# Kernel tuning notes

Hardware: AMD Instinct MI355X
Metric: run time of the kernel (lower is better)

Reference implementation:

```python
import jax, jax.numpy as jnp
import numpy as np

# dims: Q queries, K hops (topk), N relation groups, M padded nodes/group
Q, K, N, M = 64, 2, 32, 64
E, D, R, S = 256, 1024, 200, 8192  # embs_size, model_size, n_rel, seq positions


def setup_inputs() -> dict:
    key = jax.random.key(0)
    ks = jax.random.split(key, 10)
    hidden_states = jax.random.normal(ks[0], (S, D), jnp.float32)
    nodes = jax.random.normal(ks[1], (Q, K, N, M, E), jnp.float32)
    # ragged groups: zero-pad beyond a random valid length (mirrors F.pad + stack)
    lengths = jax.random.randint(ks[2], (Q, K, N), 1, M + 1)
    valid = jnp.arange(M)[None, None, None, :] < lengths[..., None]
    nodes = nodes * valid[..., None]
    prob_idx = jax.random.randint(ks[3], (Q, K, N), 0, R)
    gnn_idx = jnp.arange(Q, dtype=jnp.int32)          # gnn_mask positions
    rel_idx = jnp.arange(Q, dtype=jnp.int32) + Q      # rel_mask positions (disjoint)
    sc = lambda fan: float(1.0 / np.sqrt(fan))
    u = lambda k, shp, fan: jax.random.uniform(k, shp, jnp.float32, -sc(fan), sc(fan))
    Wc = u(ks[4], (D, R), D); bc = jnp.zeros((R,), jnp.float32)
    Wq = u(ks[5], (D, D), D); bq = jnp.zeros((D,), jnp.float32)
    Wn = u(ks[6], (E, D), E); bn = jnp.zeros((D,), jnp.float32)
    Wg = u(ks[7], (E, D), E); bg = jnp.zeros((D,), jnp.float32)
    return {"hidden_states": hidden_states, "nodes": nodes, "prob_idx": prob_idx,
            "gnn_idx": gnn_idx, "rel_idx": rel_idx,
            "Wc": Wc, "bc": bc, "Wq": Wq, "bq": bq,
            "Wn": Wn, "bn": bn, "Wg": Wg, "bg": bg}


def reference(hidden_states, nodes, prob_idx, gnn_idx, rel_idx,
              Wc, bc, Wq, bq, Wn, bn, Wg, bg):
    Qn, Kn, Nn, Mn, En = nodes.shape
    # classification_head: Linear + Softmax over relations
    rel_prob = jax.nn.softmax(hidden_states[rel_idx] @ Wc + bc, axis=1)  # [Q,R]
    # gather per-group relation probabilities (extract_values_from_tensor)
    probs = jnp.take_along_axis(rel_prob, prob_idx.reshape(Qn, Kn * Nn), axis=1)
    probs = probs.reshape(Qn, Kn, Nn)                                     # [Q,K,N]
    # mask from first feature of padded node embeddings (as in calculate_scores)
    mask = nodes[..., 0] != 0                                             # [Q,K,N,M]
    # query_reprj and nodes_reprj (Linear + Tanh)
    gq = jnp.tanh(hidden_states[gnn_idx] @ Wq + bq)                       # [Q,D]
    gn = jnp.tanh(jnp.einsum('qknme,ed->qknmd', nodes, Wn) + bn)          # [Q,K,N,M,D]
    dots = jnp.einsum('qknmd,qd->qknm', gn, gq)                           # [Q,K,N,M]
    attn = jax.nn.softmax(dots, axis=3)            # softmax over nodes within group
    logits = attn * probs[..., None] / 0.1         # scale by group prob / temperature
    # global softmax over all (group, node) slots per (query, hop)
    wa = jax.nn.softmax(logits.reshape(Qn, Kn, Nn * Mn), axis=-1)
    wa = wa.reshape(Qn, Kn, Nn, Mn)
    wa = jnp.where(mask, wa, 0.0)
    # weighted mean over the flattened N*M slots, then mean over topk hops
    mean_emb = jnp.mean(nodes * wa[..., None], axis=(2, 3))               # [Q,K,E]
    pooled = mean_emb.mean(axis=1)                                        # [Q,E]
    out = jnp.tanh(pooled @ Wg + bg)                                      # gnn_reprj
    return hidden_states.at[gnn_idx].add(out)
```

## Files before the change

### kernel.cpp

```cpp
#include <hip/hip_runtime.h>
#include <hip/hip_bf16.h>
#include <math.h>

#define QDIM 64
#define KDIM 2
#define NDIM 32
#define MDIM 64
#define EDIM 256
#define DDIM 1024
#define RDIM 200
#define SDIM 8192
#define GCOUNT (QDIM * KDIM * NDIM)

typedef short short8_t __attribute__((ext_vector_type(8)));
typedef float f32x4 __attribute__((ext_vector_type(4)));

__device__ __forceinline__ float tanh_c(float x) {
    float e = __expf(2.0f * x);
    return 1.0f - 2.0f * __builtin_amdgcn_rcpf(1.0f + e);
}

__device__ __forceinline__ uint32_t f2bf(float f) {
    uint32_t u = __float_as_uint(f);
    return (u + 0x7fffu + ((u >> 16) & 1u)) >> 16;
}
__device__ __forceinline__ float bf2f(uint16_t h) {
    return __uint_as_float(((uint32_t)h) << 16);
}

__global__ __launch_bounds__(256) void prologue_kernel(
    const float* __restrict__ hs, float* __restrict__ out,
    const float* __restrict__ Wn, short* __restrict__ wnpk,
    const int* __restrict__ gnn_idx, const float* __restrict__ Wq,
    const float* __restrict__ bq, float* __restrict__ gqo,
    const int* __restrict__ rel_idx, const float* __restrict__ Wc,
    const float* __restrict__ bc, float* __restrict__ rel_prob,
    const float* __restrict__ nodes, int* __restrict__ nvarr) {
    const int b = blockIdx.x, t = threadIdx.x;
    __shared__ float row[DDIM];
    __shared__ float arr[256];

    if (b < 2048) {
        const float4* src = (const float4*)hs;
        float4* dst = (float4*)out;
        int i = b * 256 + t;
#pragma unroll
        for (int r = 0; r < 4; ++r) dst[i + r * 524288] = src[i + r * 524288];
    } else if (b < 2176) {
        int tid = (b - 2048) * 256 + t;
        int lane = tid & 63, ks = (tid >> 6) & 7, ntg = tid >> 9;
        int low = lane & 15, hi = lane >> 4;
        short8_t o;
#pragma unroll
        for (int j = 0; j < 8; ++j) {
            int k = ks * 32 + hi * 8 + j;
            int d = ntg * 16 + low;
            o[j] = (short)f2bf(Wn[(size_t)k * DDIM + d]);
        }
        *(short8_t*)(wnpk + (size_t)tid * 8) = o;
    } else if (b < 2432) {
        int bb = b - 2176;
        int q = bb >> 2, seg = bb & 3;
        const float* src = hs + (size_t)gnn_idx[q] * DDIM;
        for (int i = t; i < DDIM; i += 256) row[i] = src[i];
        __syncthreads();
        int d = seg * 256 + t;
        float a = bq[d];
#pragma unroll 8
        for (int k = 0; k < DDIM; ++k) a += row[k] * Wq[(size_t)k * DDIM + d];
        gqo[(size_t)q * DDIM + d] = tanh_c(a);
    } else if (b < 2496) {
        int q = b - 2432;
        const float* src = hs + (size_t)rel_idx[q] * DDIM;
        for (int i = t; i < DDIM; i += 256) row[i] = src[i];
        __syncthreads();
        float lg = -INFINITY;
        if (t < RDIM) {
            float a = bc[t];
            for (int k = 0; k < DDIM; ++k) a += row[k] * Wc[(size_t)k * RDIM + t];
            lg = a;
        }
        arr[t] = lg;
        __syncthreads();
        for (int s = 128; s > 0; s >>= 1) {
            if (t < s) arr[t] = fmaxf(arr[t], arr[t + s]);
            __syncthreads();
        }
        float mx = arr[0];
        __syncthreads();
        float ex = (t < RDIM) ? __expf(lg - mx) : 0.0f;
        arr[t] = ex;
        __syncthreads();
        for (int s = 128; s > 0; s >>= 1) {
            if (t < s) arr[t] += arr[t + s];
            __syncthreads();
        }
        float sm = arr[0];
        if (t < RDIM) rel_prob[q * RDIM + t] = ex / sm;
    } else {
        int g = (b - 2496) * 4 + (t >> 6);
        int lane = t & 63;
        float f0 = nodes[(size_t)g * (MDIM * EDIM) + (size_t)lane * EDIM];
        unsigned long long mk = __ballot(f0 != 0.0f);
        if (lane == 0) nvarr[g] = __popcll(mk);
    }
}

struct SharedBufs {
    alignas(16) char ldsbuf[MDIM * EDIM * 2];
    float part[4][MDIM];
    float cqp[4];
    float lv[MDIM];
};

template <int MT>
__device__ __forceinline__ void phase1_body(
    SharedBufs* sb, int g, int q, const float* __restrict__ nodes,
    const short* __restrict__ wnpk, const float* __restrict__ bn,
    const float* __restrict__ gq, const float* __restrict__ rel_prob,
    const int* __restrict__ prob_idx, float* __restrict__ gvec,
    float* __restrict__ gden, float* __restrict__ gmx) {
    const int t = threadIdx.x;
    const int lane = t & 63, w = t >> 6;
    const int low = lane & 15, hi = lane >> 4;
    constexpr int NS = MT * 16;
    constexpr int TAIL = 64 - NS;

    {
        const float4* src = (const float4*)(nodes + (size_t)g * (MDIM * EDIM));
#pragma unroll
        for (int i = 0; i < MT * 4; ++i) {
            int idx4 = i * 256 + t;
            float4 v = src[idx4];
            int m = idx4 >> 6;
            int byteoff = (m * 512 + (idx4 & 63) * 8) ^ ((m & 7) << 4);
            uint32_t w0 = f2bf(v.x) | (f2bf(v.y) << 16);
            uint32_t w1 = f2bf(v.z) | (f2bf(v.w) << 16);
            *(uint2*)(sb->ldsbuf + byteoff) = make_uint2(w0, w1);
        }
    }
    __syncthreads();

    short8_t af[MT][8];
#pragma unroll
    for (int mt = 0; mt < MT; ++mt)
#pragma unroll
        for (int ks = 0; ks < 8; ++ks) {
            int rrow = mt * 16 + low;
            int byteoff = (rrow * 512 + ks * 64 + hi * 16) ^ ((low & 7) << 4);
            af[mt][ks] = *(const short8_t*)(sb->ldsbuf + byteoff);
        }

    float dacc[MT][4];
#pragma unroll
    for (int mt = 0; mt < MT; ++mt)
#pragma unroll
        for (int jj = 0; jj < 4; ++jj) dacc[mt][jj] = 0.f;

    float cpart = 0.f;
    const float* gqrow = gq + (size_t)q * DDIM;
    for (int nt = 0; nt < 16; ++nt) {
        const int ntg = w * 16 + nt;
        const int d = ntg * 16 + low;
        float gqv = gqrow[d];
        float bnv = bn[d];
        cpart += tanh_c(bnv) * gqv;
        f32x4 acc[MT];
#pragma unroll
        for (int mt = 0; mt < MT; ++mt) acc[mt] = (f32x4){0.f, 0.f, 0.f, 0.f};
        const short8_t* bp = (const short8_t*)(wnpk) + ((size_t)ntg * 8 * 64 + lane);
#pragma unroll
        for (int ks = 0; ks < 8; ++ks) {
            short8_t bf = bp[ks * 64];
#pragma unroll
            for (int mt = 0; mt < MT; ++mt)
                acc[mt] = __builtin_amdgcn_mfma_f32_16x16x32_bf16(af[mt][ks], bf, acc[mt], 0, 0, 0);
        }
#pragma unroll
        for (int mt = 0; mt < MT; ++mt)
#pragma unroll
            for (int jj = 0; jj < 4; ++jj)
                dacc[mt][jj] += tanh_c(acc[mt][jj] + bnv) * gqv;
    }

#pragma unroll
    for (int mt = 0; mt < MT; ++mt)
#pragma unroll
        for (int jj = 0; jj < 4; ++jj) {
            float v = dacc[mt][jj];
            v += __shfl_xor(v, 1);
            v += __shfl_xor(v, 2);
            v += __shfl_xor(v, 4);
            v += __shfl_xor(v, 8);
            if (low == 0) sb->part[w][mt * 16 + hi * 4 + jj] = v;
        }
    {
        float cw = cpart;
#pragma unroll
        for (int off = 32; off > 0; off >>= 1) cw += __shfl_xor(cw, off);
        if (lane == 0) sb->cqp[w] = cw;
    }
    __syncthreads();

    if (t < 64) {
        float cq = 0.25f * (sb->cqp[0] + sb->cqp[1] + sb->cqp[2] + sb->cqp[3]);
        float dv = (t < NS) ? (sb->part[0][t] + sb->part[1][t] + sb->part[2][t] + sb->part[3][t])
                            : -INFINITY;
        float mx = dv;
#pragma unroll
        for (int off = 32; off > 0; off >>= 1) mx = fmaxf(mx, __shfl_xor(mx, off));
        if (TAIL > 0) mx = fmaxf(mx, cq);
        float ex = (t < NS) ? __expf(dv - mx) : 0.0f;
        float sm = ex;
#pragma unroll
        for (int off = 32; off > 0; off >>= 1) sm += __shfl_xor(sm, off);
        float ext = __expf(cq - mx);
        sm += (float)TAIL * ext;
        float pr = rel_prob[(size_t)q * RDIM + prob_idx[g]];
        float attn = ex / sm;
        float lgv = (t < NS) ? attn * pr * 10.0f : -INFINITY;
        float lgvt = (ext / sm) * pr * 10.0f;
        float gm = lgv;
#pragma unroll
        for (int off = 32; off > 0; off >>= 1) gm = fmaxf(gm, __shfl_xor(gm, off));
        if (TAIL > 0) gm = fmaxf(gm, lgvt);
        float el = (t < NS) ? __expf(lgv - gm) : 0.0f;
        float den = el;
#pragma unroll
        for (int off = 32; off > 0; off >>= 1) den += __shfl_xor(den, off);
        den += (float)TAIL * __expf(lgvt - gm);
        if (t < NS) {
            unsigned short raw =
                *(const unsigned short*)(sb->ldsbuf + ((t * 512) ^ ((t & 7) << 4)));
            float msk = ((raw & 0x7fffu) != 0) ? 1.0f : 0.0f;
            sb->lv[t] = el * msk;
        }
        if (t == 0) { gden[g] = den; gmx[g] = gm; }
    }
    __syncthreads();

    float v = 0.f;
#pragma unroll 8
    for (int m = 0; m < NS; ++m) {
        unsigned short raw =
            *(const unsigned short*)(sb->ldsbuf + ((m * 512 + t * 2) ^ ((m & 7) << 4)));
        v += bf2f(raw) * sb->lv[m];
    }
    gvec[(size_t)g * EDIM + t] = v;
}

__global__ __launch_bounds__(256, 2) void phase1_mfma(
    const float* __restrict__ nodes, const short* __restrict__ wnpk,
    const float* __restrict__ bn, const float* __restrict__ gq,
    const float* __restrict__ rel_prob, const int* __restrict__ prob_idx,
    const int* __restrict__ nvarr, float* __restrict__ gvec,
    float* __restrict__ gden, float* __restrict__ gmx) {
    __shared__ SharedBufs sb;
    const int g = blockIdx.x;
    const int q = g / (KDIM * NDIM);
    int nv = nvarr[g];
    int mtiles = (nv + 15) >> 4;
    if (mtiles < 1) mtiles = 1;
    switch (mtiles) {
        case 1: phase1_body<1>(&sb, g, q, nodes, wnpk, bn, gq, rel_prob, prob_idx, gvec, gden, gmx); break;
        case 2: phase1_body<2>(&sb, g, q, nodes, wnpk, bn, gq, rel_prob, prob_idx, gvec, gden, gmx); break;
        case 3: phase1_body<3>(&sb, g, q, nodes, wnpk, bn, gq, rel_prob, prob_idx, gvec, gden, gmx); break;
        default: phase1_body<4>(&sb, g, q, nodes, wnpk, bn, gq, rel_prob, prob_idx, gvec, gden, gmx); break;
    }
}

__global__ __launch_bounds__(256) void combine_kernel(const float* __restrict__ gvec,
                                                      const float* __restrict__ gden,
                                                      const float* __restrict__ gmx,
                                                      float* __restrict__ memb) {
    int qk = blockIdx.x, t = threadIdx.x;
    __shared__ float sgm[NDIM], sden[NDIM];
    if (t < NDIM) {
        sgm[t] = gmx[qk * NDIM + t];
        sden[t] = gden[qk * NDIM + t];
    }
    __syncthreads();
    float gm = -INFINITY;
    for (int n = 0; n < NDIM; ++n) gm = fmaxf(gm, sgm[n]);
    float gs = 0.f;
    for (int n = 0; n < NDIM; ++n) gs += sden[n] * __expf(sgm[n] - gm);
    float me = 0.f;
    for (int n = 0; n < NDIM; ++n)
        me += gvec[(size_t)(qk * NDIM + n) * EDIM + t] * __expf(sgm[n] - gm);
    memb[(size_t)qk * EDIM + t] = me / (gs * (float)(NDIM * MDIM));
}

__global__ __launch_bounds__(256) void out_kernel(const float* __restrict__ memb,
                                                  const float* __restrict__ Wg,
                                                  const float* __restrict__ bg,
                                                  const int* __restrict__ gnn_idx,
                                                  float* __restrict__ out) {
    int q = blockIdx.x, t = threadIdx.x;
    __shared__ float pooled[EDIM];
    pooled[t] = 0.5f * (memb[(size_t)(q * 2 + 0) * EDIM + t] + memb[(size_t)(q * 2 + 1) * EDIM + t]);
    __syncthreads();
    float4 a = ((const float4*)bg)[t];
    const float4* Wg4 = (const float4*)Wg;
    for (int e = 0; e < EDIM; ++e) {
        float p = pooled[e];
        float4 w = Wg4[(size_t)e * (DDIM / 4) + t];
        a.x += p * w.x; a.y += p * w.y; a.z += p * w.z; a.w += p * w.w;
    }
    float4* op = (float4*)(out + (size_t)gnn_idx[q] * DDIM);
    float4 cur = op[t];
    cur.x += tanh_c(a.x);
    cur.y += tanh_c(a.y);
    cur.z += tanh_c(a.z);
    cur.w += tanh_c(a.w);
    op[t] = cur;
}

extern "C" void kernel_launch(void* const* d_in, const int* in_sizes, int n_in,
                              void* d_out, int out_size, void* d_ws, size_t ws_size,
                              hipStream_t stream) {
    const float* hs = (const float*)d_in[0];
    const float* nodes = (const float*)d_in[1];
    const int* prob_idx = (const int*)d_in[2];
    const int* gnn_idx = (const int*)d_in[3];
    const int* rel_idx = (const int*)d_in[4];
    const float* Wc = (const float*)d_in[5];
    const float* bc = (const float*)d_in[6];
    const float* Wq = (const float*)d_in[7];
    const float* bq = (const float*)d_in[8];
    const float* Wn = (const float*)d_in[9];
    const float* bn = (const float*)d_in[10];
    const float* Wg = (const float*)d_in[11];
    const float* bg = (const float*)d_in[12];
    float* out = (float*)d_out;
    float* ws = (float*)d_ws;

    float* relprob = ws;
    float* gqbuf = ws + 16384;
    float* gvec = gqbuf + (size_t)QDIM * DDIM;
    float* gdenA = gvec + (size_t)GCOUNT * EDIM;
    float* gmaxA = gdenA + GCOUNT;
    float* membuf = gmaxA + GCOUNT;
    short* wnpk = (short*)(membuf + (size_t)QDIM * KDIM * EDIM);
    int* nvarr = (int*)(wnpk + (size_t)EDIM * DDIM);

    prologue_kernel<<<3520, 256, 0, stream>>>(hs, out, Wn, wnpk, gnn_idx, Wq, bq,
                                              gqbuf, rel_idx, Wc, bc, relprob,
                                              nodes, nvarr);
    phase1_mfma<<<GCOUNT, 256, 0, stream>>>(nodes, wnpk, bn, gqbuf, relprob, prob_idx,
                                            nvarr, gvec, gdenA, gmaxA);
    combine_kernel<<<QDIM * KDIM, 256, 0, stream>>>(gvec, gdenA, gmaxA, membuf);
    out_kernel<<<QDIM, 256, 0, stream>>>(membuf, Wg, bg, gnn_idx, out);
}
```

Before: 270.6 us.

## Process one group per wavefront and bucket groups by tile count

Each group is now handled by a single 64-lane wavefront rather than a full 256-thread block. Every wave loops over all 64 D-tiles itself, so the block-level syncs and cross-wave LDS reductions go away. A new scatter kernel uses atomics to sort groups by their valid-node tile count, so the four waves in a block run the same template path and diverge less. The cost is four times as much per-wave MFMA work on Wn, plus an extra kernel launch and a memset. It also relies on an LDS ordering that uses only s_waitcnt and no barrier within the wave.

```diff
diff --git a/kernel.cpp b/kernel.cpp
--- a/kernel.cpp
+++ b/kernel.cpp
@@ -24,7 +24,7 @@
     uint32_t u = __float_as_uint(f);
     return (u + 0x7fffu + ((u >> 16) & 1u)) >> 16;
 }
-__device__ __forceinline__ float bf2f(uint16_t h) {
+__device__ __forceinline__ float bf2f(unsigned short h) {
     return __uint_as_float(((uint32_t)h) << 16);
 }
 
@@ -35,7 +35,8 @@
     const float* __restrict__ bq, float* __restrict__ gqo,
     const int* __restrict__ rel_idx, const float* __restrict__ Wc,
     const float* __restrict__ bc, float* __restrict__ rel_prob,
-    const float* __restrict__ nodes, int* __restrict__ nvarr) {
+    const float* __restrict__ nodes, int* __restrict__ nvarr,
+    int* __restrict__ bkt) {
     const int b = blockIdx.x, t = threadIdx.x;
     __shared__ float row[DDIM];
     __shared__ float arr[256];
@@ -102,73 +103,86 @@
         int lane = t & 63;
         float f0 = nodes[(size_t)g * (MDIM * EDIM) + (size_t)lane * EDIM];
         unsigned long long mk = __ballot(f0 != 0.0f);
-        if (lane == 0) nvarr[g] = __popcll(mk);
-    }
-}
-
-struct SharedBufs {
-    alignas(16) char ldsbuf[MDIM * EDIM * 2];
-    float part[4][MDIM];
-    float cqp[4];
-    float lv[MDIM];
-};
+        if (lane == 0) {
+            int nv = __popcll(mk);
+            nvarr[g] = nv;
+            int mt = (nv + 15) >> 4;
+            if (mt < 1) mt = 1;
+            atomicAdd(&bkt[mt - 1], 1);
+        }
+    }
+}
+
+__global__ __launch_bounds__(256) void scatter_kernel(const int* __restrict__ nvarr,
+                                                      int* __restrict__ bkt,
+                                                      int* __restrict__ glist) {
+    int g = blockIdx.x * 256 + threadIdx.x;
+    int nv = nvarr[g];
+    int mt = (nv + 15) >> 4;
+    if (mt < 1) mt = 1;
+    int base = 0;
+#pragma unroll
+    for (int k = 0; k < 3; ++k)
+        if (k < mt - 1) base += bkt[k];
+    int pos = base + atomicAdd(&bkt[4 + (mt - 1)], 1);
+    glist[pos] = g | (mt << 16);
+}
+
+#define WREG 9216
 
 template <int MT>
-__device__ __forceinline__ void phase1_body(
-    SharedBufs* sb, int g, int q, const float* __restrict__ nodes,
+__device__ __forceinline__ void wave_body(
+    char* ldsw, int g, int q, const float* __restrict__ nodes,
     const short* __restrict__ wnpk, const float* __restrict__ bn,
     const float* __restrict__ gq, const float* __restrict__ rel_prob,
     const int* __restrict__ prob_idx, float* __restrict__ gvec,
     float* __restrict__ gden, float* __restrict__ gmx) {
-    const int t = threadIdx.x;
-    const int lane = t & 63, w = t >> 6;
+    const int lane = threadIdx.x & 63;
     const int low = lane & 15, hi = lane >> 4;
-    constexpr int NS = MT * 16;
-    constexpr int TAIL = 64 - NS;
-
+    constexpr int NS = MT * 16, TAIL = 64 - NS;
+
+    short8_t af[MT][8];
     {
         const float4* src = (const float4*)(nodes + (size_t)g * (MDIM * EDIM));
 #pragma unroll
-        for (int i = 0; i < MT * 4; ++i) {
-            int idx4 = i * 256 + t;
-            float4 v = src[idx4];
-            int m = idx4 >> 6;
-            int byteoff = (m * 512 + (idx4 & 63) * 8) ^ ((m & 7) << 4);
-            uint32_t w0 = f2bf(v.x) | (f2bf(v.y) << 16);
-            uint32_t w1 = f2bf(v.z) | (f2bf(v.w) << 16);
-            *(uint2*)(sb->ldsbuf + byteoff) = make_uint2(w0, w1);
-        }
-    }
-    __syncthreads();
-
-    short8_t af[MT][8];
-#pragma unroll
-    for (int mt = 0; mt < MT; ++mt)
-#pragma unroll
-        for (int ks = 0; ks < 8; ++ks) {
-            int rrow = mt * 16 + low;
-            int byteoff = (rrow * 512 + ks * 64 + hi * 16) ^ ((low & 7) << 4);
-            af[mt][ks] = *(const short8_t*)(sb->ldsbuf + byteoff);
-        }
+        for (int mt = 0; mt < MT; ++mt) {
+#pragma unroll
+            for (int i = 0; i < 16; ++i) {
+                int idx4 = i * 64 + lane;
+                float4 v = src[mt * 1024 + idx4];
+                int r = idx4 >> 6, c4 = idx4 & 63;
+                int off = (r * 512 + c4 * 8) ^ ((r & 7) << 4);
+                uint32_t w0 = f2bf(v.x) | (f2bf(v.y) << 16);
+                uint32_t w1 = f2bf(v.z) | (f2bf(v.w) << 16);
+                *(uint2*)(ldsw + off) = make_uint2(w0, w1);
+            }
+            asm volatile("s_waitcnt lgkmcnt(0)" ::: "memory");
+#pragma unroll
+            for (int ks = 0; ks < 8; ++ks) {
+                int off = (low * 512 + ks * 64 + hi * 16) ^ ((low & 7) << 4);
+                af[mt][ks] = *(const short8_t*)(ldsw + off);
+            }
+            asm volatile("s_waitcnt lgkmcnt(0)" ::: "memory");
+        }
+    }
 
     float dacc[MT][4];
 #pragma unroll
     for (int mt = 0; mt < MT; ++mt)
 #pragma unroll
         for (int jj = 0; jj < 4; ++jj) dacc[mt][jj] = 0.f;
-
     float cpart = 0.f;
     const float* gqrow = gq + (size_t)q * DDIM;
-    for (int nt = 0; nt < 16; ++nt) {
-        const int ntg = w * 16 + nt;
-        const int d = ntg * 16 + low;
+    const short8_t* bb = (const short8_t*)wnpk + lane;
+    for (int ntg = 0; ntg < 64; ++ntg) {
+        int d = ntg * 16 + low;
         float gqv = gqrow[d];
         float bnv = bn[d];
         cpart += tanh_c(bnv) * gqv;
         f32x4 acc[MT];
 #pragma unroll
         for (int mt = 0; mt < MT; ++mt) acc[mt] = (f32x4){0.f, 0.f, 0.f, 0.f};
-        const short8_t* bp = (const short8_t*)(wnpk) + ((size_t)ntg * 8 * 64 + lane);
+        const short8_t* bp = bb + (size_t)ntg * 512;
 #pragma unroll
         for (int ks = 0; ks < 8; ++ks) {
             short8_t bf = bp[ks * 64];
@@ -192,80 +206,141 @@
             v += __shfl_xor(v, 2);
             v += __shfl_xor(v, 4);
             v += __shfl_xor(v, 8);
-            if (low == 0) sb->part[w][mt * 16 + hi * 4 + jj] = v;
-        }
+            dacc[mt][jj] = v;
+        }
+    float cq;
     {
         float cw = cpart;
 #pragma unroll
         for (int off = 32; off > 0; off >>= 1) cw += __shfl_xor(cw, off);
-        if (lane == 0) sb->cqp[w] = cw;
-    }
-    __syncthreads();
-
-    if (t < 64) {
-        float cq = 0.25f * (sb->cqp[0] + sb->cqp[1] + sb->cqp[2] + sb->cqp[3]);
-        float dv = (t < NS) ? (sb->part[0][t] + sb->part[1][t] + sb->part[2][t] + sb->part[3][t])
-                            : -INFINITY;
-        float mx = dv;
-#pragma unroll
-        for (int off = 32; off > 0; off >>= 1) mx = fmaxf(mx, __shfl_xor(mx, off));
-        if (TAIL > 0) mx = fmaxf(mx, cq);
-        float ex = (t < NS) ? __expf(dv - mx) : 0.0f;
-        float sm = ex;
-#pragma unroll
-        for (int off = 32; off > 0; off >>= 1) sm += __shfl_xor(sm, off);
-        float ext = __expf(cq - mx);
-        sm += (float)TAIL * ext;
-        float pr = rel_prob[(size_t)q * RDIM + prob_idx[g]];
-        float attn = ex / sm;
-        float lgv = (t < NS) ? attn * pr * 10.0f : -INFINITY;
-        float lgvt = (ext / sm) * pr * 10.0f;
-        float gm = lgv;
-#pragma unroll
-        for (int off = 32; off > 0; off >>= 1) gm = fmaxf(gm, __shfl_xor(gm, off));
-        if (TAIL > 0) gm = fmaxf(gm, lgvt);
-        float el = (t < NS) ? __expf(lgv - gm) : 0.0f;
-        float den = el;
-#pragma unroll
-        for (int off = 32; off > 0; off >>= 1) den += __shfl_xor(den, off);
-        den += (float)TAIL * __expf(lgvt - gm);
-        if (t < NS) {
-            unsigned short raw =
-                *(const unsigned short*)(sb->ldsbuf + ((t * 512) ^ ((t & 7) << 4)));
-            float msk = ((raw & 0x7fffu) != 0) ? 1.0f : 0.0f;
-            sb->lv[t] = el * msk;
-        }
-        if (t == 0) { gden[g] = den; gmx[g] = gm; }
-    }
-    __syncthreads();
-
-    float v = 0.f;
-#pragma unroll 8
-    for (int m = 0; m < NS; ++m) {
-        unsigned short raw =
-            *(const unsigned short*)(sb->ldsbuf + ((m * 512 + t * 2) ^ ((m & 7) << 4)));
-        v += bf2f(raw) * sb->lv[m];
-    }
-    gvec[(size_t)g * EDIM + t] = v;
+        cq = 0.25f * cw;
+    }
+
+    float mx = dacc[0][0];
+#pragma unroll
+    for (int mt = 0; mt < MT; ++mt)
+#pragma unroll
+        for (int jj = 0; jj < 4; ++jj) mx = fmaxf(mx, dacc[mt][jj]);
+    mx = fmaxf(mx, __shfl_xor(mx, 16));
+    mx = fmaxf(mx, __shfl_xor(mx, 32));
+    if (TAIL > 0) mx = fmaxf(mx, cq);
+    float ex[MT][4];
+    float sm = 0.f;
+#pragma unroll
+    for (int mt = 0; mt < MT; ++mt)
+#pragma unroll
+        for (int jj = 0; jj < 4; ++jj) {
+            ex[mt][jj] = __expf(dacc[mt][jj] - mx);
+            sm += ex[mt][jj];
+        }
+    sm += __shfl_xor(sm, 16);
+    sm += __shfl_xor(sm, 32);
+    float ext = __expf(cq - mx);
+    if (TAIL > 0) sm += (float)TAIL * ext;
+    float pr = rel_prob[(size_t)q * RDIM + prob_idx[g]];
+    float p10 = pr * 10.0f / sm;
+#pragma unroll
+    for (int mt = 0; mt < MT; ++mt)
+#pragma unroll
+        for (int jj = 0; jj < 4; ++jj) ex[mt][jj] *= p10;
+    float lgvt = ext * p10;
+    float gm = ex[0][0];
+#pragma unroll
+    for (int mt = 0; mt < MT; ++mt)
+#pragma unroll
+        for (int jj = 0; jj < 4; ++jj) gm = fmaxf(gm, ex[mt][jj]);
+    gm = fmaxf(gm, __shfl_xor(gm, 16));
+    gm = fmaxf(gm, __shfl_xor(gm, 32));
+    if (TAIL > 0) gm = fmaxf(gm, lgvt);
+    float el[MT][4];
+    float den = 0.f;
+#pragma unroll
+    for (int mt = 0; mt < MT; ++mt)
+#pragma unroll
+        for (int jj = 0; jj < 4; ++jj) {
+            el[mt][jj] = __expf(ex[mt][jj] - gm);
+            den += el[mt][jj];
+        }
+    den += __shfl_xor(den, 16);
+    den += __shfl_xor(den, 32);
+    if (TAIL > 0) den += (float)TAIL * __expf(lgvt - gm);
+    if (lane == 0) {
+        gden[g] = den;
+        gmx[g] = gm;
+    }
+
+    float* lvarr = (float*)(ldsw + 8192);
+    float* mkarr = lvarr + 64;
+#pragma unroll
+    for (int mt = 0; mt < MT; ++mt)
+#pragma unroll
+        for (int jj = 0; jj < 4; ++jj) lvarr[mt * 16 + hi * 4 + jj] = el[mt][jj];
+    if (hi == 0) {
+#pragma unroll
+        for (int mt = 0; mt < MT; ++mt) {
+            unsigned short s0 = (unsigned short)af[mt][0][0];
+            mkarr[mt * 16 + low] = ((s0 & 0x7fffu) != 0) ? 1.0f : 0.0f;
+        }
+    }
+    asm volatile("s_waitcnt lgkmcnt(0)" ::: "memory");
+    float lvm[MT];
+#pragma unroll
+    for (int mt = 0; mt < MT; ++mt) lvm[mt] = lvarr[mt * 16 + low] * mkarr[mt * 16 + low];
+    asm volatile("s_waitcnt lgkmcnt(0)" ::: "memory");
+
+    float ac[8][8];
+#pragma unroll
+    for (int ks = 0; ks < 8; ++ks)
+#pragma unroll
+        for (int j = 0; j < 8; ++j) ac[ks][j] = 0.f;
+#pragma unroll
+    for (int mt = 0; mt < MT; ++mt) {
+        float lw = lvm[mt];
+#pragma unroll
+        for (int ks = 0; ks < 8; ++ks)
+#pragma unroll
+            for (int j = 0; j < 8; ++j)
+                ac[ks][j] += bf2f((unsigned short)af[mt][ks][j]) * lw;
+    }
+#pragma unroll
+    for (int ks = 0; ks < 8; ++ks)
+#pragma unroll
+        for (int j = 0; j < 8; ++j) {
+            float a = ac[ks][j];
+            a += __shfl_xor(a, 1);
+            a += __shfl_xor(a, 2);
+            a += __shfl_xor(a, 4);
+            a += __shfl_xor(a, 8);
+            ac[ks][j] = a;
+        }
+    float* vb = lvarr;
+#pragma unroll
+    for (int ks = 0; ks < 8; ++ks)
+#pragma unroll
+        for (int j = 0; j < 8; ++j) vb[ks * 32 + hi * 8 + j] = ac[ks][j];
+    asm volatile("s_waitcnt lgkmcnt(0)" ::: "memory");
+    float4 ov = ((const float4*)vb)[lane];
+    *(float4*)(gvec + (size_t)g * EDIM + lane * 4) = ov;
 }
 
 __global__ __launch_bounds__(256, 2) void phase1_mfma(
     const float* __restrict__ nodes, const short* __restrict__ wnpk,
     const float* __restrict__ bn, const float* __restrict__ gq,
     const float* __restrict__ rel_prob, const int* __restrict__ prob_idx,
-    const int* __restrict__ nvarr, float* __restrict__ gvec,
+    const int* __restrict__ glist, float* __restrict__ gvec,
     float* __restrict__ gden, float* __restrict__ gmx) {
-    __shared__ SharedBufs sb;
-    const int g = blockIdx.x;
-    const int q = g / (KDIM * NDIM);
-    int nv = nvarr[g];
-    int mtiles = (nv + 15) >> 4;
-    if (mtiles < 1) mtiles = 1;
-    switch (mtiles) {
-        case 1: phase1_body<1>(&sb, g, q, nodes, wnpk, bn, gq, rel_prob, prob_idx, gvec, gden, gmx); break;
-        case 2: phase1_body<2>(&sb, g, q, nodes, wnpk, bn, gq, rel_prob, prob_idx, gvec, gden, gmx); break;
-        case 3: phase1_body<3>(&sb, g, q, nodes, wnpk, bn, gq, rel_prob, prob_idx, gvec, gden, gmx); break;
-        default: phase1_body<4>(&sb, g, q, nodes, wnpk, bn, gq, rel_prob, prob_idx, gvec, gden, gmx); break;
+    __shared__ char lds[4 * WREG];
+    int w = threadIdx.x >> 6;
+    int pk = glist[blockIdx.x * 4 + w];
+    int g = pk & 0xFFFF;
+    int mt = pk >> 16;
+    int q = g >> 6;
+    char* ldsw = lds + w * WREG;
+    switch (mt) {
+        case 1: wave_body<1>(ldsw, g, q, nodes, wnpk, bn, gq, rel_prob, prob_idx, gvec, gden, gmx); break;
+        case 2: wave_body<2>(ldsw, g, q, nodes, wnpk, bn, gq, rel_prob, prob_idx, gvec, gden, gmx); break;
+        case 3: wave_body<3>(ldsw, g, q, nodes, wnpk, bn, gq, rel_prob, prob_idx, gvec, gden, gmx); break;
+        default: wave_body<4>(ldsw, g, q, nodes, wnpk, bn, gq, rel_prob, prob_idx, gvec, gden, gmx); break;
     }
 }
 
@@ -342,12 +417,16 @@
     float* membuf = gmaxA + GCOUNT;
     short* wnpk = (short*)(membuf + (size_t)QDIM * KDIM * EDIM);
     int* nvarr = (int*)(wnpk + (size_t)EDIM * DDIM);
-
+    int* bkt = nvarr + GCOUNT;
+    int* glist = bkt + 8;
+
+    hipMemsetAsync(bkt, 0, 8 * sizeof(int), stream);
     prologue_kernel<<<3520, 256, 0, stream>>>(hs, out, Wn, wnpk, gnn_idx, Wq, bq,
                                               gqbuf, rel_idx, Wc, bc, relprob,
-                                              nodes, nvarr);
-    phase1_mfma<<<GCOUNT, 256, 0, stream>>>(nodes, wnpk, bn, gqbuf, relprob, prob_idx,
-                                            nvarr, gvec, gdenA, gmaxA);
+                                              nodes, nvarr, bkt);
+    scatter_kernel<<<GCOUNT / 256, 256, 0, stream>>>(nvarr, bkt, glist);
+    phase1_mfma<<<GCOUNT / 4, 256, 0, stream>>>(nodes, wnpk, bn, gqbuf, relprob,
+                                                prob_idx, glist, gvec, gdenA, gmaxA);
     combine_kernel<<<QDIM * KDIM, 256, 0, stream>>>(gvec, gdenA, gmaxA, membuf);
     out_kernel<<<QDIM, 256, 0, stream>>>(membuf, Wg, bg, gnn_idx, out);
 }
```

Measured after the change: 319.8 us. 1.18x slower.
